# Kernel optimization log

Hardware: AMD Instinct MI355X
Metric: run time of the kernel (lower is better)

Reference implementation:

```python
import jax, jax.numpy as jnp
import numpy as np

D = 1024      # model_dim
H = 2048      # expert hidden_dim
E = 8         # num routed experts
TOP_K = 2
N_SHARED = 1
B, S = 2, 1024


def setup_inputs() -> dict:
    key = jax.random.key(0)
    ks = jax.random.split(key, 12)
    sc = 0.02
    return {
        "hidden": jax.random.normal(ks[0], (B, S, D), jnp.float32),
        # router Linear(D -> E); stored as [in, out]
        "router_w": jax.random.normal(ks[1], (D, E), jnp.float32) * sc,
        "router_b": jnp.zeros((E,), jnp.float32),
        # shared expert (1): Linear(D->H), Linear(H->D)
        "sw1": jax.random.normal(ks[2], (D, H), jnp.float32) * sc,
        "sb1": jnp.zeros((H,), jnp.float32),
        "sw2": jax.random.normal(ks[3], (H, D), jnp.float32) * sc,
        "sb2": jnp.zeros((D,), jnp.float32),
        # routed experts, stacked over E
        "rw1": jax.random.normal(ks[4], (E, D, H), jnp.float32) * sc,
        "rb1": jnp.zeros((E, H), jnp.float32),
        "rw2": jax.random.normal(ks[5], (E, H, D), jnp.float32) * sc,
        "rb2": jnp.zeros((E, D), jnp.float32),
    }


def reference(hidden, router_w, router_b, sw1, sb1, sw2, sb2, rw1, rb1, rw2, rb2):
    b, s, d = hidden.shape
    T = b * s
    flat = hidden.reshape(T, d)                              # [T, D]

    # --- router ---
    router_logits = flat @ router_w + router_b               # [T, E]
    router_probs = jax.nn.softmax(router_logits, axis=-1)
    topk_probs, topk_idx = jax.lax.top_k(router_probs, TOP_K)  # [T, K]

    # per-(token, expert) mixing weight: sum of top-k probs that hit expert e
    weights = jnp.zeros_like(router_probs).at[
        jnp.arange(T)[:, None], topk_idx
    ].add(topk_probs)                                        # [T, E]

    # --- shared expert(s) (1 expert -> mean == itself) ---
    sh = jax.nn.gelu(flat @ sw1 + sb1, approximate=False)    # [T, H]
    shared_out = (sh @ sw2 + sb2) / N_SHARED                 # [T, D]

    # --- routed experts: dense all-expert eval weighted by routing weights ---
    # (identical math to the gather/FFN/index_add loop: weight is 0 for
    #  tokens not routed to expert e)
    h1 = jax.nn.gelu(jnp.einsum('td,edh->teh', flat, rw1) + rb1[None],
                     approximate=False)                      # [T, E, H]
    expert_out = jnp.einsum('teh,ehd->ted', h1, rw2) + rb2[None]  # [T, E, D]
    mixed = jnp.einsum('ted,te->td', expert_out, weights)    # [T, D]

    return (shared_out + mixed).reshape(b, s, d)
```

## Files before the change

kernel.cpp:

```cpp
#include <hip/hip_runtime.h>
#include <hip/hip_bf16.h>

#define T_TOK 2048
#define DDIM  1024
#define HDIM  2048
#define NEXP  8
#define NSEG  9

typedef unsigned short u16;
typedef __attribute__((ext_vector_type(4))) float f32x4;
typedef __attribute__((ext_vector_type(8))) short bf16x8;
typedef __attribute__((ext_vector_type(4))) unsigned short u16x4;

__device__ __forceinline__ u16 f2bf(float x) {
  union { float f; unsigned int u; } v; v.f = x;
  unsigned int r = v.u + 0x7fffu + ((v.u >> 16) & 1u);
  return (u16)(r >> 16);
}
__device__ __forceinline__ float gelu_exact(float x) {
  return 0.5f * x * (1.0f + erff(x * 0.70710678118654752f));
}
__device__ __forceinline__ int swz4(int row) {
  return (row & 3) ^ ((row >> 2) & 3);
}

__device__ __forceinline__ void gload16(const void* g, void* l) {
  __builtin_amdgcn_global_load_lds(
      (const __attribute__((address_space(1))) unsigned int*)g,
      (__attribute__((address_space(3))) unsigned int*)l, 16, 0, 0);
}

__global__ __launch_bounds__(256) void router_kernel(
    const float* __restrict__ x, const float* __restrict__ rw,
    const float* __restrict__ rb, u16* __restrict__ xb,
    float* __restrict__ weights, int* __restrict__ counts,
    int* __restrict__ lists)
{
  int wv = threadIdx.x >> 6, lane = threadIdx.x & 63;
  int t = blockIdx.x * 4 + wv;
  const float* xrow = x + (size_t)t * DDIM;
  float acc[NEXP];
#pragma unroll
  for (int e = 0; e < NEXP; e++) acc[e] = 0.f;
#pragma unroll
  for (int i = 0; i < 4; i++) {
    int d0 = i * 256 + lane * 4;
    f32x4 xv = *(const f32x4*)(xrow + d0);
    u16x4 pk;
#pragma unroll
    for (int j = 0; j < 4; j++) {
      float xs = xv[j];
      pk[j] = f2bf(xs);
      const float* wr = rw + (size_t)(d0 + j) * NEXP;
#pragma unroll
      for (int e = 0; e < NEXP; e++) acc[e] = fmaf(xs, wr[e], acc[e]);
    }
    *(u16x4*)(xb + (size_t)t * DDIM + d0) = pk;
  }
#pragma unroll
  for (int off = 32; off >= 1; off >>= 1)
#pragma unroll
    for (int e = 0; e < NEXP; e++) acc[e] += __shfl_xor(acc[e], off);

  if (lane == 0) {
    float lg[NEXP], mx = -1e30f;
#pragma unroll
    for (int e = 0; e < NEXP; e++) { lg[e] = acc[e] + rb[e]; mx = fmaxf(mx, lg[e]); }
    float p[NEXP], s = 0.f;
#pragma unroll
    for (int e = 0; e < NEXP; e++) { p[e] = expf(lg[e] - mx); s += p[e]; }
    float inv = 1.0f / s;
#pragma unroll
    for (int e = 0; e < NEXP; e++) p[e] *= inv;
    int i1 = 0;
#pragma unroll
    for (int e = 1; e < NEXP; e++) if (p[e] > p[i1]) i1 = e;
    int i2 = (i1 == 0) ? 1 : 0;
#pragma unroll
    for (int e = 0; e < NEXP; e++) if (e != i1 && p[e] > p[i2]) i2 = e;
#pragma unroll
    for (int e = 0; e < NEXP; e++)
      weights[(size_t)t * NEXP + e] = (e == i1) ? p[i1] : (e == i2) ? p[i2] : 0.f;
    int p1 = atomicAdd(counts + i1, 1); lists[i1 * T_TOK + p1] = t;
    int p2 = atomicAdd(counts + i2, 1); lists[i2 * T_TOK + p2] = t;
    lists[NEXP * T_TOK + t] = t;
  }
}

__global__ void seg_kernel(int* counts, int* segoff, int* ytab, int* nyt) {
  counts[NEXP] = T_TOK;
  int off = 0, n = 0;
  for (int e = 0; e < NSEG; e++) {
    segoff[e] = off;
    int c = counts[e];
    for (int my = 0; my * 256 < c; my++) ytab[n++] = e * 256 + my;
    off += c;
  }
  *nyt = n;
}


__global__ __launch_bounds__(512) void gemm1_kernel(
    const u16* __restrict__ Xb, const float* __restrict__ rw1,
    const float* __restrict__ sw1, const float* __restrict__ rb1,
    const float* __restrict__ sb1, const int* __restrict__ counts,
    const int* __restrict__ segoff, const int* __restrict__ lists,
    const int* __restrict__ ytab, const int* __restrict__ nyt,
    u16* __restrict__ H1)
{
  __shared__ u16 Alds[4][256 * 32];
  __shared__ u16 Blds[2][256 * 32];

  int tid = threadIdx.x, lane = tid & 63;
  int wv = tid >> 6, wm = wv >> 2, wn = wv & 3;
  int kc = lane >> 4, lr = lane & 15;

  int srow[2], soff[2];
#pragma unroll
  for (int j = 0; j < 2; j++) {
    int i = j * 512 + tid;
    srow[j] = i >> 2;
    soff[j] = (((i & 3) ^ swz4(i >> 2)) * 8);
  }
  int aoff[8], boff[4];
#pragma unroll
  for (int f = 0; f < 8; f++) {
    int ra = wm * 128 + f * 16 + lr;
    aoff[f] = ra * 32 + ((kc ^ swz4(ra)) * 8);
  }
#pragma unroll
  for (int f = 0; f < 4; f++) {
    int rb_ = wn * 64 + f * 16 + lr;
    boff[f] = rb_ * 32 + ((kc ^ swz4(rb_)) * 8);
  }
  int bw[4];
#pragma unroll
  for (int j = 0; j < 4; j++)
    bw[j] = ((lane << 2) + j) * 32 + (((wv >> 1) ^ j ^ (lane & 3)) << 3) + ((wv & 1) << 2);

  int ntile = nyt[0] * (HDIM / 256);
  for (int t = blockIdx.x; t < ntile; t += gridDim.x) {
    int yt = t >> 3, nx = t & 7;
    int em = ytab[yt];
    int e = em >> 8, m0 = (em & 255) * 256, n0 = nx * 256;
    int cnt = counts[e];
    const float* Wf = (e < NEXP) ? (rw1 + (size_t)e * DDIM * HDIM) : sw1;
    const float* bias = (e < NEXP) ? (rb1 + (size_t)e * HDIM) : sb1;
    const int* list = lists + e * T_TOK;
    int seg = segoff[e];

    size_t abase[2];
#pragma unroll
    for (int j = 0; j < 2; j++) {
      int tok = list[min(m0 + srow[j], cnt - 1)];
      abase[j] = (size_t)tok * DDIM + soff[j];
    }
    const float* Wb = Wf + n0 + (lane << 2);

    f32x4 acc[8][4];
#pragma unroll
    for (int i = 0; i < 8; i++)
#pragma unroll
      for (int j = 0; j < 4; j++) acc[i][j] = (f32x4){0.f, 0.f, 0.f, 0.f};

    const int NS = DDIM / 32;
    f32x4 vBa, vBb, vBc, vBd;
    {
      const float* Wk = Wb + (size_t)(wv * 4) * HDIM;
      vBa = *(const f32x4*)(Wk);
      vBb = *(const f32x4*)(Wk + HDIM);
      vBc = *(const f32x4*)(Wk + 2 * HDIM);
      vBd = *(const f32x4*)(Wk + 3 * HDIM);
    }
#pragma unroll
    for (int s = 0; s < 2; s++)
#pragma unroll
      for (int j = 0; j < 2; j++) {
        int i = j * 512 + tid;
        gload16(Xb + abase[j] + s * 32, &Alds[s][i * 8]);
      }

    for (int s = 0; s < NS; s++) {
      if (s + 2 < NS) {
        int kk = (s + 2) * 32;
        int nb = (s + 2) & 3;
#pragma unroll
        for (int j = 0; j < 2; j++) {
          int i = j * 512 + tid;
          gload16(Xb + abase[j] + kk, &Alds[nb][i * 8]);
        }
      }
      {
        u16* Bd = &Blds[s & 1][0];
#pragma unroll
        for (int j = 0; j < 4; j++) {
          u16x4 pk;
          pk[0] = f2bf(vBa[j]); pk[1] = f2bf(vBb[j]);
          pk[2] = f2bf(vBc[j]); pk[3] = f2bf(vBd[j]);
          *(u16x4*)(Bd + bw[j]) = pk;
        }
      }
      if (s + 1 < NS) {
        const float* Wk = Wb + (size_t)((s + 1) * 32 + wv * 4) * HDIM;
        vBa = *(const f32x4*)(Wk);
        vBb = *(const f32x4*)(Wk + HDIM);
        vBc = *(const f32x4*)(Wk + 2 * HDIM);
        vBd = *(const f32x4*)(Wk + 3 * HDIM);
      }
      if (s + 2 < NS)      asm volatile("s_waitcnt vmcnt(8)" ::: "memory");
      else if (s + 1 < NS) asm volatile("s_waitcnt vmcnt(6)" ::: "memory");
      else                 asm volatile("s_waitcnt vmcnt(0)" ::: "memory");
      asm volatile("s_waitcnt lgkmcnt(0)" ::: "memory");
      __builtin_amdgcn_s_barrier();
      __builtin_amdgcn_sched_barrier(0);

      const u16* Ac = &Alds[s & 3][0];
      const u16* Bc = &Blds[s & 1][0];
      bf16x8 af[8], bfr[4];
#pragma unroll
      for (int f = 0; f < 8; f++) af[f] = *(const bf16x8*)(Ac + aoff[f]);
#pragma unroll
      for (int f = 0; f < 4; f++) bfr[f] = *(const bf16x8*)(Bc + boff[f]);
      __builtin_amdgcn_s_setprio(1);
#pragma unroll
      for (int mf = 0; mf < 8; mf++)
#pragma unroll
        for (int nf = 0; nf < 4; nf++)
          acc[mf][nf] = __builtin_amdgcn_mfma_f32_16x16x32_bf16(af[mf], bfr[nf], acc[mf][nf], 0, 0, 0);
      __builtin_amdgcn_s_setprio(0);
    }

#pragma unroll
    for (int nf = 0; nf < 4; nf++) {
      int col = n0 + wn * 64 + nf * 16 + lr;
      float b = bias[col];
#pragma unroll
      for (int mf = 0; mf < 8; mf++) {
#pragma unroll
        for (int rg = 0; rg < 4; rg++) {
          int mt = wm * 128 + mf * 16 + kc * 4 + rg;
          if (m0 + mt < cnt) {
            float v = acc[mf][nf][rg] + b;
            H1[(size_t)(seg + m0 + mt) * HDIM + col] = f2bf(gelu_exact(v));
          }
        }
      }
    }
    __builtin_amdgcn_s_barrier();
    __builtin_amdgcn_sched_barrier(0);
  }
}

__global__ __launch_bounds__(512) void gemm2_kernel(
    const u16* __restrict__ H1, const float* __restrict__ rw2,
    const float* __restrict__ sw2, const float* __restrict__ rb2,
    const float* __restrict__ sb2, const float* __restrict__ weights,
    const int* __restrict__ counts, const int* __restrict__ segoff,
    const int* __restrict__ lists, const int* __restrict__ ytab,
    const int* __restrict__ nyt, float* __restrict__ out)
{
  __shared__ u16 Alds[4][256 * 32];
  __shared__ u16 Blds[2][256 * 32];

  int tid = threadIdx.x, lane = tid & 63;
  int wv = tid >> 6, wm = wv >> 2, wn = wv & 3;
  int kc = lane >> 4, lr = lane & 15;

  int srow[2], soff[2];
#pragma unroll
  for (int j = 0; j < 2; j++) {
    int i = j * 512 + tid;
    srow[j] = i >> 2;
    soff[j] = (((i & 3) ^ swz4(i >> 2)) * 8);
  }
  int aoff[8], boff[4];
#pragma unroll
  for (int f = 0; f < 8; f++) {
    int ra = wm * 128 + f * 16 + lr;
    aoff[f] = ra * 32 + ((kc ^ swz4(ra)) * 8);
  }
#pragma unroll
  for (int f = 0; f < 4; f++) {
    int rb_ = wn * 64 + f * 16 + lr;
    boff[f] = rb_ * 32 + ((kc ^ swz4(rb_)) * 8);
  }
  int bw[4];
#pragma unroll
  for (int j = 0; j < 4; j++)
    bw[j] = ((lane << 2) + j) * 32 + (((wv >> 1) ^ j ^ (lane & 3)) << 3) + ((wv & 1) << 2);

  int ntile = nyt[0] * (DDIM / 256) * 2;
  for (int t = blockIdx.x; t < ntile; t += gridDim.x) {
    int kh = t & 1, nx = (t >> 1) & 3, yt = t >> 3;
    int em = ytab[yt];
    int e = em >> 8, m0 = (em & 255) * 256, n0 = nx * 256;
    int cnt = counts[e];
    const float* Wf = (e < NEXP) ? (rw2 + (size_t)e * HDIM * DDIM) : sw2;
    const float* bias = (e < NEXP) ? (rb2 + (size_t)e * DDIM) : sb2;
    const int* list = lists + e * T_TOK;
    int seg = segoff[e];
    int k0 = kh * 1024;

    size_t abase[2];
#pragma unroll
    for (int j = 0; j < 2; j++)
      abase[j] = (size_t)(seg + min(m0 + srow[j], cnt - 1)) * HDIM + k0 + soff[j];
    const float* Wb = Wf + (size_t)k0 * DDIM + n0 + (lane << 2);

    f32x4 acc[8][4];
#pragma unroll
    for (int i = 0; i < 8; i++)
#pragma unroll
      for (int j = 0; j < 4; j++) acc[i][j] = (f32x4){0.f, 0.f, 0.f, 0.f};

    const int NS = 1024 / 32;
    f32x4 vBa, vBb, vBc, vBd;
    {
      const float* Wk = Wb + (size_t)(wv * 4) * DDIM;
      vBa = *(const f32x4*)(Wk);
      vBb = *(const f32x4*)(Wk + DDIM);
      vBc = *(const f32x4*)(Wk + 2 * DDIM);
      vBd = *(const f32x4*)(Wk + 3 * DDIM);
    }
#pragma unroll
    for (int s = 0; s < 2; s++)
#pragma unroll
      for (int j = 0; j < 2; j++) {
        int i = j * 512 + tid;
        gload16(H1 + abase[j] + s * 32, &Alds[s][i * 8]);
      }

    for (int s = 0; s < NS; s++) {
      if (s + 2 < NS) {
        int kk = (s + 2) * 32;
        int nb = (s + 2) & 3;
#pragma unroll
        for (int j = 0; j < 2; j++) {
          int i = j * 512 + tid;
          gload16(H1 + abase[j] + kk, &Alds[nb][i * 8]);
        }
      }
      {
        u16* Bd = &Blds[s & 1][0];
#pragma unroll
        for (int j = 0; j < 4; j++) {
          u16x4 pk;
          pk[0] = f2bf(vBa[j]); pk[1] = f2bf(vBb[j]);
          pk[2] = f2bf(vBc[j]); pk[3] = f2bf(vBd[j]);
          *(u16x4*)(Bd + bw[j]) = pk;
        }
      }
      if (s + 1 < NS) {
        const float* Wk = Wb + (size_t)((s + 1) * 32 + wv * 4) * DDIM;
        vBa = *(const f32x4*)(Wk);
        vBb = *(const f32x4*)(Wk + DDIM);
        vBc = *(const f32x4*)(Wk + 2 * DDIM);
        vBd = *(const f32x4*)(Wk + 3 * DDIM);
      }
      if (s + 2 < NS)      asm volatile("s_waitcnt vmcnt(8)" ::: "memory");
      else if (s + 1 < NS) asm volatile("s_waitcnt vmcnt(6)" ::: "memory");
      else                 asm volatile("s_waitcnt vmcnt(0)" ::: "memory");
      asm volatile("s_waitcnt lgkmcnt(0)" ::: "memory");
      __builtin_amdgcn_s_barrier();
      __builtin_amdgcn_sched_barrier(0);

      const u16* Ac = &Alds[s & 3][0];
      const u16* Bc = &Blds[s & 1][0];
      bf16x8 af[8], bfr[4];
#pragma unroll
      for (int f = 0; f < 8; f++) af[f] = *(const bf16x8*)(Ac + aoff[f]);
#pragma unroll
      for (int f = 0; f < 4; f++) bfr[f] = *(const bf16x8*)(Bc + boff[f]);
      __builtin_amdgcn_s_setprio(1);
#pragma unroll
      for (int mf = 0; mf < 8; mf++)
#pragma unroll
        for (int nf = 0; nf < 4; nf++)
          acc[mf][nf] = __builtin_amdgcn_mfma_f32_16x16x32_bf16(af[mf], bfr[nf], acc[mf][nf], 0, 0, 0);
      __builtin_amdgcn_s_setprio(0);
    }

    float biasv[4];
#pragma unroll
    for (int nf = 0; nf < 4; nf++)
      biasv[nf] = (kh == 0) ? bias[n0 + wn * 64 + nf * 16 + lr] : 0.f;

#pragma unroll
    for (int mf = 0; mf < 8; mf++) {
#pragma unroll
      for (int rg = 0; rg < 4; rg++) {
        int mt = wm * 128 + mf * 16 + kc * 4 + rg;
        int mrow = m0 + mt;
        if (mrow < cnt) {
          int tok = list[mrow];
          float w = (e < NEXP) ? weights[(size_t)tok * NEXP + e] : 1.0f;
          float* orow = out + (size_t)tok * DDIM + n0 + wn * 64 + lr;
#pragma unroll
          for (int nf = 0; nf < 4; nf++)
            atomicAdd(orow + nf * 16, w * (acc[mf][nf][rg] + biasv[nf]));
        }
      }
    }
    __builtin_amdgcn_s_barrier();
    __builtin_amdgcn_sched_barrier(0);
  }
}

extern "C" void kernel_launch(void* const* d_in, const int* in_sizes, int n_in,
                              void* d_out, int out_size, void* d_ws, size_t ws_size,
                              hipStream_t stream) {
  (void)in_sizes; (void)n_in; (void)out_size; (void)ws_size;
  const float* hidden   = (const float*)d_in[0];
  const float* router_w = (const float*)d_in[1];
  const float* router_b = (const float*)d_in[2];
  const float* sw1 = (const float*)d_in[3];
  const float* sb1 = (const float*)d_in[4];
  const float* sw2 = (const float*)d_in[5];
  const float* sb2 = (const float*)d_in[6];
  const float* rw1 = (const float*)d_in[7];
  const float* rb1 = (const float*)d_in[8];
  const float* rw2 = (const float*)d_in[9];
  const float* rb2 = (const float*)d_in[10];
  float* out = (float*)d_out;

  char* ws = (char*)d_ws;
  u16* Xb      = (u16*)(ws + 0);
  u16* H1      = (u16*)(ws + 4194304);
  float* weights = (float*)(ws + 29360128);
  int* counts  = (int*)(ws + 29425664);
  int* segoff  = (int*)(ws + 29425728);
  int* lists   = (int*)(ws + 29425792);
  int* ytab    = (int*)(ws + 29499520);
  int* nyt     = (int*)(ws + 29500160);

  hipMemsetAsync(counts, 0, 64, stream);
  hipMemsetAsync(out, 0, (size_t)T_TOK * DDIM * sizeof(float), stream);

  router_kernel<<<T_TOK / 4, 256, 0, stream>>>(hidden, router_w, router_b, Xb,
                                               weights, counts, lists);
  seg_kernel<<<1, 1, 0, stream>>>(counts, segoff, ytab, nyt);

  gemm1_kernel<<<256, 512, 0, stream>>>(
      Xb, rw1, sw1, rb1, sb1, counts, segoff, lists, ytab, nyt, H1);
  gemm2_kernel<<<256, 512, 0, stream>>>(
      H1, rw2, sw2, rb2, sb2, weights, counts, segoff, lists, ytab, nyt, out);
}
```

Baseline: 229.3 us.

## Prefetch B weights one extra stage and remap tiles contiguously per XCD

```diff
diff --git a/kernel.cpp b/kernel.cpp
--- a/kernel.cpp
+++ b/kernel.cpp
@@ -138,9 +138,16 @@
   for (int j = 0; j < 4; j++)
     bw[j] = ((lane << 2) + j) * 32 + (((wv >> 1) ^ j ^ (lane & 3)) << 3) + ((wv & 1) << 2);
 
-  int ntile = nyt[0] * (HDIM / 256);
-  for (int t = blockIdx.x; t < ntile; t += gridDim.x) {
-    int yt = t >> 3, nx = t & 7;
+  int nyt0 = nyt[0];
+  int ntile = nyt0 * (HDIM / 256);
+  int q = ntile >> 3, rm = ntile & 7;
+  int xcd = blockIdx.x & 7, bidx = blockIdx.x >> 3, bstr = gridDim.x >> 3;
+  int start = (xcd < rm) ? xcd * (q + 1) : rm * (q + 1) + (xcd - rm) * q;
+  int cntx = q + ((xcd < rm) ? 1 : 0);
+
+  for (int p = bidx; p < cntx; p += bstr) {
+    int u = start + p;
+    int nx = u / nyt0, yt = u - nx * nyt0;
     int em = ytab[yt];
     int e = em >> 8, m0 = (em & 255) * 256, n0 = nx * 256;
     int cnt = counts[e];
@@ -179,6 +186,23 @@
         int i = j * 512 + tid;
         gload16(Xb + abase[j] + s * 32, &Alds[s][i * 8]);
       }
+    {
+      u16* Bd = &Blds[0][0];
+#pragma unroll
+      for (int j = 0; j < 4; j++) {
+        u16x4 pk;
+        pk[0] = f2bf(vBa[j]); pk[1] = f2bf(vBb[j]);
+        pk[2] = f2bf(vBc[j]); pk[3] = f2bf(vBd[j]);
+        *(u16x4*)(Bd + bw[j]) = pk;
+      }
+    }
+    {
+      const float* Wk = Wb + (size_t)(32 + wv * 4) * HDIM;
+      vBa = *(const f32x4*)(Wk);
+      vBb = *(const f32x4*)(Wk + HDIM);
+      vBc = *(const f32x4*)(Wk + 2 * HDIM);
+      vBd = *(const f32x4*)(Wk + 3 * HDIM);
+    }
 
     for (int s = 0; s < NS; s++) {
       if (s + 2 < NS) {
@@ -189,9 +213,18 @@
           int i = j * 512 + tid;
           gload16(Xb + abase[j] + kk, &Alds[nb][i * 8]);
         }
-      }
-      {
-        u16* Bd = &Blds[s & 1][0];
+        asm volatile("s_waitcnt vmcnt(8)" ::: "memory");
+      } else if (s + 1 < NS) {
+        asm volatile("s_waitcnt vmcnt(6)" ::: "memory");
+      } else {
+        asm volatile("s_waitcnt vmcnt(0)" ::: "memory");
+      }
+      asm volatile("s_waitcnt lgkmcnt(0)" ::: "memory");
+      __builtin_amdgcn_s_barrier();
+      __builtin_amdgcn_sched_barrier(0);
+
+      if (s + 1 < NS) {
+        u16* Bd = &Blds[(s + 1) & 1][0];
 #pragma unroll
         for (int j = 0; j < 4; j++) {
           u16x4 pk;
@@ -199,20 +232,14 @@
           pk[2] = f2bf(vBc[j]); pk[3] = f2bf(vBd[j]);
           *(u16x4*)(Bd + bw[j]) = pk;
         }
-      }
-      if (s + 1 < NS) {
-        const float* Wk = Wb + (size_t)((s + 1) * 32 + wv * 4) * HDIM;
-        vBa = *(const f32x4*)(Wk);
-        vBb = *(const f32x4*)(Wk + HDIM);
-        vBc = *(const f32x4*)(Wk + 2 * HDIM);
-        vBd = *(const f32x4*)(Wk + 3 * HDIM);
-      }
-      if (s + 2 < NS)      asm volatile("s_waitcnt vmcnt(8)" ::: "memory");
-      else if (s + 1 < NS) asm volatile("s_waitcnt vmcnt(6)" ::: "memory");
-      else                 asm volatile("s_waitcnt vmcnt(0)" ::: "memory");
-      asm volatile("s_waitcnt lgkmcnt(0)" ::: "memory");
-      __builtin_amdgcn_s_barrier();
-      __builtin_amdgcn_sched_barrier(0);
+        if (s + 2 < NS) {
+          const float* Wk = Wb + (size_t)((s + 2) * 32 + wv * 4) * HDIM;
+          vBa = *(const f32x4*)(Wk);
+          vBb = *(const f32x4*)(Wk + HDIM);
+          vBc = *(const f32x4*)(Wk + 2 * HDIM);
+          vBd = *(const f32x4*)(Wk + 3 * HDIM);
+        }
+      }
 
       const u16* Ac = &Alds[s & 3][0];
       const u16* Bc = &Blds[s & 1][0];
@@ -289,9 +316,17 @@
   for (int j = 0; j < 4; j++)
     bw[j] = ((lane << 2) + j) * 32 + (((wv >> 1) ^ j ^ (lane & 3)) << 3) + ((wv & 1) << 2);
 
-  int ntile = nyt[0] * (DDIM / 256) * 2;
-  for (int t = blockIdx.x; t < ntile; t += gridDim.x) {
-    int kh = t & 1, nx = (t >> 1) & 3, yt = t >> 3;
+  int nyt0 = nyt[0];
+  int ntile = nyt0 * (DDIM / 256) * 2;
+  int q = ntile >> 3, rm = ntile & 7;
+  int xcd = blockIdx.x & 7, bidx = blockIdx.x >> 3, bstr = gridDim.x >> 3;
+  int start = (xcd < rm) ? xcd * (q + 1) : rm * (q + 1) + (xcd - rm) * q;
+  int cntx = q + ((xcd < rm) ? 1 : 0);
+
+  for (int p = bidx; p < cntx; p += bstr) {
+    int u = start + p;
+    int panel = u / nyt0, yt = u - panel * nyt0;
+    int kh = panel & 1, nx = panel >> 1;
     int em = ytab[yt];
     int e = em >> 8, m0 = (em & 255) * 256, n0 = nx * 256;
     int cnt = counts[e];
@@ -329,6 +364,23 @@
         int i = j * 512 + tid;
         gload16(H1 + abase[j] + s * 32, &Alds[s][i * 8]);
       }
+    {
+      u16* Bd = &Blds[0][0];
+#pragma unroll
+      for (int j = 0; j < 4; j++) {
+        u16x4 pk;
+        pk[0] = f2bf(vBa[j]); pk[1] = f2bf(vBb[j]);
+        pk[2] = f2bf(vBc[j]); pk[3] = f2bf(vBd[j]);
+        *(u16x4*)(Bd + bw[j]) = pk;
+      }
+    }
+    {
+      const float* Wk = Wb + (size_t)(32 + wv * 4) * DDIM;
+      vBa = *(const f32x4*)(Wk);
+      vBb = *(const f32x4*)(Wk + DDIM);
+      vBc = *(const f32x4*)(Wk + 2 * DDIM);
+      vBd = *(const f32x4*)(Wk + 3 * DDIM);
+    }
 
     for (int s = 0; s < NS; s++) {
       if (s + 2 < NS) {
@@ -339,9 +391,18 @@
           int i = j * 512 + tid;
           gload16(H1 + abase[j] + kk, &Alds[nb][i * 8]);
         }
-      }
-      {
-        u16* Bd = &Blds[s & 1][0];
+        asm volatile("s_waitcnt vmcnt(8)" ::: "memory");
+      } else if (s + 1 < NS) {
+        asm volatile("s_waitcnt vmcnt(6)" ::: "memory");
+      } else {
+        asm volatile("s_waitcnt vmcnt(0)" ::: "memory");
+      }
+      asm volatile("s_waitcnt lgkmcnt(0)" ::: "memory");
+      __builtin_amdgcn_s_barrier();
+      __builtin_amdgcn_sched_barrier(0);
+
+      if (s + 1 < NS) {
+        u16* Bd = &Blds[(s + 1) & 1][0];
 #pragma unroll
         for (int j = 0; j < 4; j++) {
           u16x4 pk;
@@ -349,20 +410,14 @@
           pk[2] = f2bf(vBc[j]); pk[3] = f2bf(vBd[j]);
           *(u16x4*)(Bd + bw[j]) = pk;
         }
-      }
-      if (s + 1 < NS) {
-        const float* Wk = Wb + (size_t)((s + 1) * 32 + wv * 4) * DDIM;
-        vBa = *(const f32x4*)(Wk);
-        vBb = *(const f32x4*)(Wk + DDIM);
-        vBc = *(const f32x4*)(Wk + 2 * DDIM);
-        vBd = *(const f32x4*)(Wk + 3 * DDIM);
-      }
-      if (s + 2 < NS)      asm volatile("s_waitcnt vmcnt(8)" ::: "memory");
-      else if (s + 1 < NS) asm volatile("s_waitcnt vmcnt(6)" ::: "memory");
-      else                 asm volatile("s_waitcnt vmcnt(0)" ::: "memory");
-      asm volatile("s_waitcnt lgkmcnt(0)" ::: "memory");
-      __builtin_amdgcn_s_barrier();
-      __builtin_amdgcn_sched_barrier(0);
+        if (s + 2 < NS) {
+          const float* Wk = Wb + (size_t)((s + 2) * 32 + wv * 4) * DDIM;
+          vBa = *(const f32x4*)(Wk);
+          vBb = *(const f32x4*)(Wk + DDIM);
+          vBc = *(const f32x4*)(Wk + 2 * DDIM);
+          vBd = *(const f32x4*)(Wk + 3 * DDIM);
+        }
+      }
 
       const u16* Ac = &Alds[s & 3][0];
       const u16* Bc = &Blds[s & 1][0];
```

Result: slower. 241.1 us (+5.1%).
